# Optimization experiments

Measured on AMD Instinct MI355X. Metric: run time of the kernel, lower is better.

Reference implementation:

```python
import jax, jax.numpy as jnp
import numpy as np

N_NODES = 50000
N_EDGES = 800000
IN_FEATS = 128
HIDDEN = 256
N_CLASSES = 64


def setup_inputs() -> dict:
    key = jax.random.key(0)
    ks = jax.random.split(key, 16)
    def w(k, shape, fan_in):
        return jax.random.normal(k, shape, dtype=jnp.float32) * (1.0 / np.sqrt(fan_in))
    inp = {
        "x": jax.random.normal(ks[0], (N_NODES, IN_FEATS), dtype=jnp.float32),
        "edge_src": jax.random.randint(ks[1], (N_EDGES,), 0, N_NODES, dtype=jnp.int32),
        "edge_dst": jax.random.randint(ks[2], (N_EDGES,), 0, N_NODES, dtype=jnp.int32),
        # layer 0: in_feats -> hidden
        "W0s": w(ks[3], (IN_FEATS, HIDDEN), IN_FEATS),
        "W0n": w(ks[4], (IN_FEATS, HIDDEN), IN_FEATS),
        "b0": jnp.zeros((HIDDEN,), dtype=jnp.float32),
        # layer 1: hidden -> hidden
        "W1s": w(ks[5], (HIDDEN, HIDDEN), HIDDEN),
        "W1n": w(ks[6], (HIDDEN, HIDDEN), HIDDEN),
        "b1": jnp.zeros((HIDDEN,), dtype=jnp.float32),
        # layer 2: hidden -> hidden (last conv also outputs hidden per source code)
        "W2s": w(ks[7], (HIDDEN, HIDDEN), HIDDEN),
        "W2n": w(ks[8], (HIDDEN, HIDDEN), HIDDEN),
        "b2": jnp.zeros((HIDDEN,), dtype=jnp.float32),
        # fc1: hidden -> n_classes
        "Wfc": w(ks[9], (HIDDEN, N_CLASSES), HIDDEN),
        "bfc": jnp.zeros((N_CLASSES,), dtype=jnp.float32),
    }
    return inp


def _sage_layer(h, src, dst, Ws, Wn, b):
    # mean-neighbor aggregation: segment-sum messages, divide by in-degree
    msg = h[src]  # [E, D] irregular gather
    agg = jax.ops.segment_sum(msg, dst, num_segments=N_NODES)  # [N, D]
    deg = jax.ops.segment_sum(jnp.ones_like(dst, dtype=h.dtype), dst, num_segments=N_NODES)
    h_neigh = agg / jnp.maximum(deg, 1.0)[:, None]
    # DGL SAGEConv (mean): fc_self(h) + fc_neigh(h_neigh) + bias
    return h @ Ws + h_neigh @ Wn + b


def reference(x, edge_src, edge_dst, W0s, W0n, b0, W1s, W1n, b1, W2s, W2n, b2, Wfc, bfc):
    # forward applies dropout (identity at eval) and NO activation between layers,
    # matching the original module's forward().
    h = _sage_layer(x, edge_src, edge_dst, W0s, W0n, b0)
    h = _sage_layer(h, edge_src, edge_dst, W1s, W1n, b1)
    h = _sage_layer(h, edge_src, edge_dst, W2s, W2n, b2)
    return h @ Wfc + bfc  # [N, n_classes]
```

## Files before the change

kernel.cpp:

```cpp
#include <hip/hip_runtime.h>

#define NN 50000
#define NE 800000
#define F_IN 128
#define HID 256
#define N_CLS 64
#define SCAN_BLOCKS ((NN + 255) / 256)
#define CROWS 515

typedef _Float16 half8 __attribute__((ext_vector_type(8)));
typedef float f32x4 __attribute__((ext_vector_type(4)));

__global__ void hist_count(const int* __restrict__ dst, int* __restrict__ cnt,
                           unsigned short* __restrict__ rank, int E) {
    int i = blockIdx.x * blockDim.x + threadIdx.x;
    if (i < E) rank[i] = (unsigned short)atomicAdd(&cnt[dst[i]], 1);
}

__device__ __forceinline__ void scan_block_sums_dev(const int* __restrict__ cnt,
                                                    int* __restrict__ blockSums, int n) {
    __shared__ int s[256];
    int t = threadIdx.x;
    int i = blockIdx.x * 256 + t;
    s[t] = (i < n) ? cnt[i] : 0;
    __syncthreads();
    for (int off = 128; off > 0; off >>= 1) {
        if (t < off) s[t] += s[t + off];
        __syncthreads();
    }
    if (t == 0) blockSums[blockIdx.x] = s[0];
}

__device__ __forceinline__ void scan_top_dev(int* __restrict__ blockSums, int nb) {
    __shared__ int s[256];
    int t = threadIdx.x;
    s[t] = (t < nb) ? blockSums[t] : 0;
    __syncthreads();
    for (int off = 1; off < 256; off <<= 1) {
        int v = (t >= off) ? s[t - off] : 0;
        __syncthreads();
        s[t] += v;
        __syncthreads();
    }
    if (t < nb) blockSums[t] = (t > 0) ? s[t - 1] : 0;
}

__device__ __forceinline__ void scan_final_dev(const int* __restrict__ cnt,
                                               const int* __restrict__ blockBase,
                                               int* __restrict__ offs,
                                               float* __restrict__ dinv, int n) {
    __shared__ int s[256];
    int t = threadIdx.x;
    int i = blockIdx.x * 256 + t;
    int v = (i < n) ? cnt[i] : 0;
    s[t] = v;
    __syncthreads();
    for (int off = 1; off < 256; off <<= 1) {
        int u = (t >= off) ? s[t - off] : 0;
        __syncthreads();
        s[t] += u;
        __syncthreads();
    }
    if (i < n) {
        offs[i] = blockBase[blockIdx.x] + s[t] - v;
        dinv[i] = 1.0f / (float)max(v, 1);
    }
    if (i == n - 1) offs[n] = blockBase[blockIdx.x] + s[t];
}

__global__ void csr_place2(const int* __restrict__ src, const int* __restrict__ dst,
                           const unsigned short* __restrict__ rank, const int* __restrict__ offs,
                           unsigned short* __restrict__ csr, int E) {
    int e = blockIdx.x * blockDim.x + threadIdx.x;
    if (e < E) csr[offs[dst[e]] + rank[e]] = (unsigned short)src[e];
}

__device__ __forceinline__ const float* virtC1_row(int r, const float* W0s,
                                                   const float* W0n, const float* b0) {
    if (r < 0) return nullptr;
    if (r < 128) return W0s + (size_t)r * 256;
    if (r < 256) return W0n + (size_t)(r - 128) * 256;
    if (r == 512) return b0;
    return nullptr;
}

__device__ __forceinline__ int shift_src(int r) {
    if (r >= 128 && r < 512) return r - 128;
    if (r == 513) return 512;
    if (r == 514) return 513;
    return -1;
}


__device__ __forceinline__ void compose_first_dev(
    int bx, const float* __restrict__ W0s, const float* __restrict__ W0n,
    const float* __restrict__ b0,
    const float* __restrict__ B1, const float* __restrict__ B2,
    const float* __restrict__ brow, float* __restrict__ C)
{
    __shared__ float As[64][17];
    __shared__ float Bs[16][64];
    const int tid = threadIdx.x;
    const int tx = tid & 15, ty = tid >> 4;
    const int row0 = (bx % 9) * 64;
    const int col0 = (bx / 9) * 64;
    const int lr = tid >> 2, lc = tid & 3;
    const int br = tid >> 4, bc = tid & 15;

    float acc[4][4] = {};

    for (int pass = 0; pass < 2; ++pass) {
        const float* B = pass ? B2 : B1;
        int grow = row0 + lr;
        int srcr = pass ? shift_src(grow) : (grow < CROWS ? grow : -1);
        const float* ap = virtC1_row(srcr, W0s, W0n, b0);

        for (int k0 = 0; k0 < 256; k0 += 16) {
            float4 av = make_float4(0.f, 0.f, 0.f, 0.f);
            if (ap) av = *(const float4*)(ap + k0 + lc * 4);
            As[lr][lc * 4 + 0] = av.x;
            As[lr][lc * 4 + 1] = av.y;
            As[lr][lc * 4 + 2] = av.z;
            As[lr][lc * 4 + 3] = av.w;
            *(float4*)&Bs[br][bc * 4] = *(const float4*)(B + (size_t)(k0 + br) * 256 + col0 + bc * 4);
            __syncthreads();
            #pragma unroll
            for (int k = 0; k < 16; ++k) {
                float a[4];
                #pragma unroll
                for (int i = 0; i < 4; ++i) a[i] = As[ty * 4 + i][k];
                float4 bv = *(const float4*)&Bs[k][tx * 4];
                const float b[4] = {bv.x, bv.y, bv.z, bv.w};
                #pragma unroll
                for (int i = 0; i < 4; ++i)
                    #pragma unroll
                    for (int j = 0; j < 4; ++j)
                        acc[i][j] += a[i] * b[j];
            }
            __syncthreads();
        }
    }

    #pragma unroll
    for (int i = 0; i < 4; ++i) {
        int r = row0 + ty * 4 + i;
        if (r < CROWS) {
            #pragma unroll
            for (int j = 0; j < 4; ++j) {
                float v = acc[i][j];
                if (r == 512) v += brow[col0 + tx * 4 + j];
                C[(size_t)r * 256 + col0 + tx * 4 + j] = v;
            }
        }
    }
}

__device__ __forceinline__ void compose_mid_dev(
    int bx, const float* __restrict__ A,
    const float* __restrict__ B1, const float* __restrict__ B2,
    const float* __restrict__ brow, float* __restrict__ C)
{
    __shared__ float As[64][17];
    __shared__ float Bs[16][64];
    const int tid = threadIdx.x;
    const int tx = tid & 15, ty = tid >> 4;
    const int row0 = (bx % 9) * 64;
    const int col0 = (bx / 9) * 64;
    const int lr = tid >> 2, lc = tid & 3;
    const int br = tid >> 4, bc = tid & 15;

    float acc[4][4] = {};

    for (int pass = 0; pass < 2; ++pass) {
        const float* B = pass ? B2 : B1;
        int grow = row0 + lr;
        int p = pass ? shift_src(grow) : (grow < CROWS ? grow : -1);

        for (int k0 = 0; k0 < 256; k0 += 16) {
            float4 av = make_float4(0.f, 0.f, 0.f, 0.f);
            if (p >= 0) av = *(const float4*)(A + (size_t)p * 256 + k0 + lc * 4);
            As[lr][lc * 4 + 0] = av.x;
            As[lr][lc * 4 + 1] = av.y;
            As[lr][lc * 4 + 2] = av.z;
            As[lr][lc * 4 + 3] = av.w;
            *(float4*)&Bs[br][bc * 4] = *(const float4*)(B + (size_t)(k0 + br) * 256 + col0 + bc * 4);
            __syncthreads();
            #pragma unroll
            for (int k = 0; k < 16; ++k) {
                float a[4];
                #pragma unroll
                for (int i = 0; i < 4; ++i) a[i] = As[ty * 4 + i][k];
                float4 bv = *(const float4*)&Bs[k][tx * 4];
                const float b[4] = {bv.x, bv.y, bv.z, bv.w};
                #pragma unroll
                for (int i = 0; i < 4; ++i)
                    #pragma unroll
                    for (int j = 0; j < 4; ++j)
                        acc[i][j] += a[i] * b[j];
            }
            __syncthreads();
        }
    }

    #pragma unroll
    for (int i = 0; i < 4; ++i) {
        int r = row0 + ty * 4 + i;
        if (r < CROWS) {
            #pragma unroll
            for (int j = 0; j < 4; ++j) {
                float v = acc[i][j];
                if (r == 512) v += brow[col0 + tx * 4 + j];
                C[(size_t)r * 256 + col0 + tx * 4 + j] = v;
            }
        }
    }
}

__device__ __forceinline__ void compose_last_dev(
    int bx, const float* __restrict__ A, const float* __restrict__ B1,
    const float* __restrict__ brow, float* __restrict__ Vf, _Float16* __restrict__ BT)
{
    __shared__ float As[64][17];
    __shared__ float Bs[16][64];
    const int tid = threadIdx.x;
    const int tx = tid & 15, ty = tid >> 4;
    const int row0 = bx * 64;
    const int lr = tid >> 2, lc = tid & 3;
    const int br = tid >> 4, bc = tid & 15;

    float acc[4][4] = {};

    for (int k0 = 0; k0 < 256; k0 += 16) {
        float4 av = make_float4(0.f, 0.f, 0.f, 0.f);
        int grow = row0 + lr;
        if (grow < CROWS) av = *(const float4*)(A + (size_t)grow * 256 + k0 + lc * 4);
        As[lr][lc * 4 + 0] = av.x;
        As[lr][lc * 4 + 1] = av.y;
        As[lr][lc * 4 + 2] = av.z;
        As[lr][lc * 4 + 3] = av.w;
        *(float4*)&Bs[br][bc * 4] = *(const float4*)(B1 + (size_t)(k0 + br) * 64 + bc * 4);
        __syncthreads();
        #pragma unroll
        for (int k = 0; k < 16; ++k) {
            float a[4];
            #pragma unroll
            for (int i = 0; i < 4; ++i) a[i] = As[ty * 4 + i][k];
            float4 bv = *(const float4*)&Bs[k][tx * 4];
            const float b[4] = {bv.x, bv.y, bv.z, bv.w};
            #pragma unroll
            for (int i = 0; i < 4; ++i)
                #pragma unroll
                for (int j = 0; j < 4; ++j)
                    acc[i][j] += a[i] * b[j];
        }
        __syncthreads();
    }

    #pragma unroll
    for (int i = 0; i < 4; ++i) {
        int r = row0 + ty * 4 + i;
        if (r < CROWS) {
            #pragma unroll
            for (int j = 0; j < 4; ++j) {
                int c = tx * 4 + j;
                float v = acc[i][j];
                if (r == 512) v += brow[c];
                Vf[(size_t)r * 64 + c] = v;
                if (r < 512)
                    BT[(size_t)((r >> 7) * 64 + c) * 128 + (r & 127)] = (_Float16)v;
            }
        }
    }
}

__global__ __launch_bounds__(256) void k_scanA_composeF(
    const int* __restrict__ cnt, int* __restrict__ blockSums,
    const float* __restrict__ W0s, const float* __restrict__ W0n, const float* __restrict__ b0,
    const float* __restrict__ W1s, const float* __restrict__ W1n, const float* __restrict__ b1,
    float* __restrict__ C2)
{
    if (blockIdx.x < SCAN_BLOCKS) scan_block_sums_dev(cnt, blockSums, NN);
    else compose_first_dev(blockIdx.x - SCAN_BLOCKS, W0s, W0n, b0, W1s, W1n, b1, C2);
}

__global__ __launch_bounds__(256) void k_scanT_composeM(
    int* __restrict__ blockSums,
    const float* __restrict__ C2,
    const float* __restrict__ W2s, const float* __restrict__ W2n, const float* __restrict__ b2,
    float* __restrict__ C3)
{
    if (blockIdx.x == 0) scan_top_dev(blockSums, SCAN_BLOCKS);
    else compose_mid_dev(blockIdx.x - 1, C2, W2s, W2n, b2, C3);
}

__global__ __launch_bounds__(256) void k_scanF_composeL(
    const int* __restrict__ cnt, const int* __restrict__ blockBase,
    int* __restrict__ offs, float* __restrict__ dinv,
    const float* __restrict__ C3, const float* __restrict__ Wfc, const float* __restrict__ bfc,
    float* __restrict__ Vf, _Float16* __restrict__ BT)
{
    if (blockIdx.x < SCAN_BLOCKS) scan_final_dev(cnt, blockBase, offs, dinv, NN);
    else compose_last_dev(blockIdx.x - SCAN_BLOCKS, C3, Wfc, bfc, Vf, BT);
}

__global__ __launch_bounds__(256) void gemm_Y(
    const float* __restrict__ X, const _Float16* __restrict__ BT,
    _Float16* __restrict__ Y, _Float16* __restrict__ Tc, int N)
{
    constexpr int LP = 40;
    __shared__ _Float16 As[128 * LP];
    __shared__ _Float16 Bs[128 * LP];

    const int tid = threadIdx.x;
    const int wave = tid >> 6;
    const int lane = tid & 63;
    const int l15 = lane & 15;
    const int quad = lane >> 4;
    const int wrow = wave >> 1;
    const int wcol = wave & 1;
    const int m_base = wrow * 64;
    const int n_base = wcol * 64;

    const int row0 = blockIdx.x * 128;
    const int col0 = blockIdx.y * 128;

    f32x4 acc[4][4] = {};

    for (int k0 = 0; k0 < 128; k0 += 32) {
        #pragma unroll
        for (int r = 0; r < 2; ++r) {
            int idx = r * 256 + tid;
            int row = idx >> 2, ch = idx & 3;
            int gr = row0 + row; if (gr > N - 1) gr = N - 1;
            const float* ap = X + (size_t)gr * 128 + k0 + ch * 8;
            float4 f0 = *(const float4*)ap;
            float4 f1 = *(const float4*)(ap + 4);
            half8 v = { (_Float16)f0.x, (_Float16)f0.y, (_Float16)f0.z, (_Float16)f0.w,
                        (_Float16)f1.x, (_Float16)f1.y, (_Float16)f1.z, (_Float16)f1.w };
            *(half8*)&As[row * LP + ch * 8] = v;
        }
        #pragma unroll
        for (int r = 0; r < 2; ++r) {
            int idx = r * 256 + tid;
            int row = idx >> 2, ch = idx & 3;
            *(half8*)&Bs[row * LP + ch * 8] =
                *(const half8*)(BT + (size_t)(col0 + row) * 128 + k0 + ch * 8);
        }
        __syncthreads();
        half8 af[4], bf[4];
        #pragma unroll
        for (int i = 0; i < 4; ++i)
            af[i] = *(const half8*)&As[(m_base + i * 16 + l15) * LP + quad * 8];
        #pragma unroll
        for (int j = 0; j < 4; ++j)
            bf[j] = *(const half8*)&Bs[(n_base + j * 16 + l15) * LP + quad * 8];
        #pragma unroll
        for (int i = 0; i < 4; ++i)
            #pragma unroll
            for (int j = 0; j < 4; ++j)
                acc[i][j] = __builtin_amdgcn_mfma_f32_16x16x32_f16(af[i], bf[j], acc[i][j], 0, 0, 0);
        __syncthreads();
    }

    #pragma unroll
    for (int i = 0; i < 4; ++i) {
        #pragma unroll
        for (int j = 0; j < 4; ++j) {
            int col = col0 + n_base + j * 16 + l15;
            #pragma unroll
            for (int r = 0; r < 4; ++r) {
                int row = row0 + m_base + i * 16 + quad * 4 + r;
                if (row < N) {
                    _Float16 v = (_Float16)acc[i][j][r];
                    Y[(size_t)row * 256 + col] = v;
                    if (col >= 192) Tc[(size_t)row * 64 + (col - 192)] = v;
                }
            }
        }
    }
}

template <bool OUT_F32>
__global__ __launch_bounds__(256) void gather64(
    const _Float16* __restrict__ Tin,
    const unsigned short* __restrict__ csr, const int* __restrict__ offs,
    const float* __restrict__ dinv,
    const _Float16* __restrict__ Yadd,
    const float* __restrict__ cvec,
    void* __restrict__ Tout, int N)
{
    int node = blockIdx.x * 32 + (threadIdx.x >> 3);
    int lane = threadIdx.x & 7;
    if (node >= N) return;
    int beg = offs[node], end = offs[node + 1];
    float acc[8] = {};
    int e = beg;
    for (; e + 3 < end; e += 4) {
        int s0 = csr[e], s1 = csr[e + 1], s2 = csr[e + 2], s3 = csr[e + 3];
        half8 v0 = *(const half8*)(Tin + (size_t)s0 * 64 + lane * 8);
        half8 v1 = *(const half8*)(Tin + (size_t)s1 * 64 + lane * 8);
        half8 v2 = *(const half8*)(Tin + (size_t)s2 * 64 + lane * 8);
        half8 v3 = *(const half8*)(Tin + (size_t)s3 * 64 + lane * 8);
        #pragma unroll
        for (int j = 0; j < 8; ++j)
            acc[j] += ((float)v0[j] + (float)v1[j]) + ((float)v2[j] + (float)v3[j]);
    }
    for (; e < end; ++e) {
        half8 v = *(const half8*)(Tin + (size_t)csr[e] * 64 + lane * 8);
        #pragma unroll
        for (int j = 0; j < 8; ++j) acc[j] += (float)v[j];
    }
    float sc = dinv[node];
    half8 y = *(const half8*)(Yadd + (size_t)node * 256 + lane * 8);
    if (OUT_F32) {
        float* o = (float*)Tout + (size_t)node * 64 + lane * 8;
        float4 o0, o1;
        o0.x = acc[0] * sc + (float)y[0] + cvec[lane * 8 + 0];
        o0.y = acc[1] * sc + (float)y[1] + cvec[lane * 8 + 1];
        o0.z = acc[2] * sc + (float)y[2] + cvec[lane * 8 + 2];
        o0.w = acc[3] * sc + (float)y[3] + cvec[lane * 8 + 3];
        o1.x = acc[4] * sc + (float)y[4] + cvec[lane * 8 + 4];
        o1.y = acc[5] * sc + (float)y[5] + cvec[lane * 8 + 5];
        o1.z = acc[6] * sc + (float)y[6] + cvec[lane * 8 + 6];
        o1.w = acc[7] * sc + (float)y[7] + cvec[lane * 8 + 7];
        *(float4*)o = o0;
        *(float4*)(o + 4) = o1;
    } else {
        half8 o;
        #pragma unroll
        for (int j = 0; j < 8; ++j)
            o[j] = (_Float16)(acc[j] * sc + (float)y[j] + cvec[lane * 8 + j]);
        *(half8*)((_Float16*)Tout + (size_t)node * 64 + lane * 8) = o;
    }
}

extern "C" void kernel_launch(void* const* d_in, const int* in_sizes, int n_in,
                              void* d_out, int out_size, void* d_ws, size_t ws_size,
                              hipStream_t stream) {
    const float* x    = (const float*)d_in[0];
    const int*   esrc = (const int*)d_in[1];
    const int*   edst = (const int*)d_in[2];
    const float* W0s  = (const float*)d_in[3];
    const float* W0n  = (const float*)d_in[4];
    const float* b0   = (const float*)d_in[5];
    const float* W1s  = (const float*)d_in[6];
    const float* W1n  = (const float*)d_in[7];
    const float* b1   = (const float*)d_in[8];
    const float* W2s  = (const float*)d_in[9];
    const float* W2n  = (const float*)d_in[10];
    const float* b2   = (const float*)d_in[11];
    const float* Wfc  = (const float*)d_in[12];
    const float* bfc  = (const float*)d_in[13];
    float* out = (float*)d_out;

    _Float16* Y   = (_Float16*)d_ws;
    _Float16* Ta  = Y + (size_t)NN * 256;
    _Float16* Tb  = Ta + (size_t)NN * 64;
    _Float16* Tc  = Tb + (size_t)NN * 64;
    _Float16* BT  = Tc + (size_t)NN * 64;
    float* C2     = (float*)(BT + 256 * 128);
    float* C3     = C2 + CROWS * 256;
    float* Vf     = C3 + CROWS * 256;
    float* dinv   = Vf + CROWS * 64;
    int* cnt      = (int*)(dinv + NN);
    int* offs     = cnt + NN;
    int* blockSums = offs + NN + 1;
    unsigned short* rank = (unsigned short*)(blockSums + SCAN_BLOCKS);
    unsigned short* csr  = rank + NE;

    hipMemsetAsync(cnt, 0, (size_t)NN * sizeof(int), stream);
    hist_count<<<(NE + 255) / 256, 256, 0, stream>>>(edst, cnt, rank, NE);
    k_scanA_composeF<<<SCAN_BLOCKS + 36, 256, 0, stream>>>(
        cnt, blockSums, W0s, W0n, b0, W1s, W1n, b1, C2);
    k_scanT_composeM<<<1 + 36, 256, 0, stream>>>(blockSums, C2, W2s, W2n, b2, C3);
    k_scanF_composeL<<<SCAN_BLOCKS + 9, 256, 0, stream>>>(
        cnt, blockSums, offs, dinv, C3, Wfc, bfc, Vf, BT);
    csr_place2<<<(NE + 255) / 256, 256, 0, stream>>>(esrc, edst, rank, offs, csr, NE);

    gemm_Y<<<dim3((NN + 127) / 128, 2), 256, 0, stream>>>(x, BT, Y, Tc, NN);

    const int ggrid = (NN + 31) / 32;
    gather64<false><<<ggrid, 256, 0, stream>>>(
        Tc, csr, offs, dinv, Y + 128, Vf + (size_t)514 * 64, Ta, NN);
    gather64<false><<<ggrid, 256, 0, stream>>>(
        Ta, csr, offs, dinv, Y + 64, Vf + (size_t)513 * 64, Tb, NN);
    gather64<true><<<ggrid, 256, 0, stream>>>(
        Tb, csr, offs, dinv, Y, Vf + (size_t)512 * 64, out, NN);
}
```

Baseline: 291.9 us.

## Reschedule setup stages into fused launches and run gathers in one cooperative kernel

Reorders the preprocessing pipeline so the histogram overlaps the first weight composition, and the scan stages overlap the remaining compose and the split GEMM. The CSR placement is merged with the second GEMM half. The three gather layers are replaced by a single cooperative grid-stride kernel with grid-wide syncs, falling back to separate launches if the cooperative launch fails. This removes several kernel launches and their boundaries, but the grid syncs and the fixed grid size (256 CUs times occupancy) may cost load balance and occupancy.

```diff
diff --git a/kernel.cpp b/kernel.cpp
--- a/kernel.cpp
+++ b/kernel.cpp
@@ -1,4 +1,7 @@
 #include <hip/hip_runtime.h>
+#include <hip/hip_cooperative_groups.h>
+
+namespace cg = cooperative_groups;
 
 #define NN 50000
 #define NE 800000
@@ -6,74 +9,14 @@
 #define HID 256
 #define N_CLS 64
 #define SCAN_BLOCKS ((NN + 255) / 256)
+#define HB ((NE + 255) / 256)
+#define CF_BLOCKS 36
+#define CL_BLOCKS 9
+#define GA_BLOCKS ((NN + 127) / 128)
 #define CROWS 515
 
 typedef _Float16 half8 __attribute__((ext_vector_type(8)));
 typedef float f32x4 __attribute__((ext_vector_type(4)));
-
-__global__ void hist_count(const int* __restrict__ dst, int* __restrict__ cnt,
-                           unsigned short* __restrict__ rank, int E) {
-    int i = blockIdx.x * blockDim.x + threadIdx.x;
-    if (i < E) rank[i] = (unsigned short)atomicAdd(&cnt[dst[i]], 1);
-}
-
-__device__ __forceinline__ void scan_block_sums_dev(const int* __restrict__ cnt,
-                                                    int* __restrict__ blockSums, int n) {
-    __shared__ int s[256];
-    int t = threadIdx.x;
-    int i = blockIdx.x * 256 + t;
-    s[t] = (i < n) ? cnt[i] : 0;
-    __syncthreads();
-    for (int off = 128; off > 0; off >>= 1) {
-        if (t < off) s[t] += s[t + off];
-        __syncthreads();
-    }
-    if (t == 0) blockSums[blockIdx.x] = s[0];
-}
-
-__device__ __forceinline__ void scan_top_dev(int* __restrict__ blockSums, int nb) {
-    __shared__ int s[256];
-    int t = threadIdx.x;
-    s[t] = (t < nb) ? blockSums[t] : 0;
-    __syncthreads();
-    for (int off = 1; off < 256; off <<= 1) {
-        int v = (t >= off) ? s[t - off] : 0;
-        __syncthreads();
-        s[t] += v;
-        __syncthreads();
-    }
-    if (t < nb) blockSums[t] = (t > 0) ? s[t - 1] : 0;
-}
-
-__device__ __forceinline__ void scan_final_dev(const int* __restrict__ cnt,
-                                               const int* __restrict__ blockBase,
-                                               int* __restrict__ offs,
-                                               float* __restrict__ dinv, int n) {
-    __shared__ int s[256];
-    int t = threadIdx.x;
-    int i = blockIdx.x * 256 + t;
-    int v = (i < n) ? cnt[i] : 0;
-    s[t] = v;
-    __syncthreads();
-    for (int off = 1; off < 256; off <<= 1) {
-        int u = (t >= off) ? s[t - off] : 0;
-        __syncthreads();
-        s[t] += u;
-        __syncthreads();
-    }
-    if (i < n) {
-        offs[i] = blockBase[blockIdx.x] + s[t] - v;
-        dinv[i] = 1.0f / (float)max(v, 1);
-    }
-    if (i == n - 1) offs[n] = blockBase[blockIdx.x] + s[t];
-}
-
-__global__ void csr_place2(const int* __restrict__ src, const int* __restrict__ dst,
-                           const unsigned short* __restrict__ rank, const int* __restrict__ offs,
-                           unsigned short* __restrict__ csr, int E) {
-    int e = blockIdx.x * blockDim.x + threadIdx.x;
-    if (e < E) csr[offs[dst[e]] + rank[e]] = (unsigned short)src[e];
-}
 
 __device__ __forceinline__ const float* virtC1_row(int r, const float* W0s,
                                                    const float* W0n, const float* b0) {
@@ -90,7 +33,6 @@
     if (r == 514) return 513;
     return -1;
 }
-
 
 __device__ __forceinline__ void compose_first_dev(
     int bx, const float* __restrict__ W0s, const float* __restrict__ W0n,
@@ -273,37 +215,59 @@
     }
 }
 
-__global__ __launch_bounds__(256) void k_scanA_composeF(
-    const int* __restrict__ cnt, int* __restrict__ blockSums,
-    const float* __restrict__ W0s, const float* __restrict__ W0n, const float* __restrict__ b0,
-    const float* __restrict__ W1s, const float* __restrict__ W1n, const float* __restrict__ b1,
-    float* __restrict__ C2)
-{
-    if (blockIdx.x < SCAN_BLOCKS) scan_block_sums_dev(cnt, blockSums, NN);
-    else compose_first_dev(blockIdx.x - SCAN_BLOCKS, W0s, W0n, b0, W1s, W1n, b1, C2);
-}
-
-__global__ __launch_bounds__(256) void k_scanT_composeM(
-    int* __restrict__ blockSums,
-    const float* __restrict__ C2,
-    const float* __restrict__ W2s, const float* __restrict__ W2n, const float* __restrict__ b2,
-    float* __restrict__ C3)
-{
-    if (blockIdx.x == 0) scan_top_dev(blockSums, SCAN_BLOCKS);
-    else compose_mid_dev(blockIdx.x - 1, C2, W2s, W2n, b2, C3);
-}
-
-__global__ __launch_bounds__(256) void k_scanF_composeL(
-    const int* __restrict__ cnt, const int* __restrict__ blockBase,
-    int* __restrict__ offs, float* __restrict__ dinv,
-    const float* __restrict__ C3, const float* __restrict__ Wfc, const float* __restrict__ bfc,
-    float* __restrict__ Vf, _Float16* __restrict__ BT)
-{
-    if (blockIdx.x < SCAN_BLOCKS) scan_final_dev(cnt, blockBase, offs, dinv, NN);
-    else compose_last_dev(blockIdx.x - SCAN_BLOCKS, C3, Wfc, bfc, Vf, BT);
-}
-
-__global__ __launch_bounds__(256) void gemm_Y(
+__device__ __forceinline__ void scan_block_sums_dev(const int* __restrict__ cnt,
+                                                    int* __restrict__ blockSums, int n, int bx) {
+    __shared__ int s[256];
+    int t = threadIdx.x;
+    int i = bx * 256 + t;
+    s[t] = (i < n) ? cnt[i] : 0;
+    __syncthreads();
+    for (int off = 128; off > 0; off >>= 1) {
+        if (t < off) s[t] += s[t + off];
+        __syncthreads();
+    }
+    if (t == 0) blockSums[bx] = s[0];
+}
+
+__device__ __forceinline__ void scan_top_dev(int* __restrict__ blockSums, int nb) {
+    __shared__ int s[256];
+    int t = threadIdx.x;
+    s[t] = (t < nb) ? blockSums[t] : 0;
+    __syncthreads();
+    for (int off = 1; off < 256; off <<= 1) {
+        int v = (t >= off) ? s[t - off] : 0;
+        __syncthreads();
+        s[t] += v;
+        __syncthreads();
+    }
+    if (t < nb) blockSums[t] = (t > 0) ? s[t - 1] : 0;
+}
+
+__device__ __forceinline__ void scan_final_dev(const int* __restrict__ cnt,
+                                               const int* __restrict__ blockBase,
+                                               int* __restrict__ offs,
+                                               float* __restrict__ dinv, int n, int bx) {
+    __shared__ int s[256];
+    int t = threadIdx.x;
+    int i = bx * 256 + t;
+    int v = (i < n) ? cnt[i] : 0;
+    s[t] = v;
+    __syncthreads();
+    for (int off = 1; off < 256; off <<= 1) {
+        int u = (t >= off) ? s[t - off] : 0;
+        __syncthreads();
+        s[t] += u;
+        __syncthreads();
+    }
+    if (i < n) {
+        offs[i] = blockBase[bx] + s[t] - v;
+        dinv[i] = 1.0f / (float)max(v, 1);
+    }
+    if (i == n - 1) offs[n] = blockBase[bx] + s[t];
+}
+
+__device__ __forceinline__ void gemm_y_dev(
+    int bx, int by,
     const float* __restrict__ X, const _Float16* __restrict__ BT,
     _Float16* __restrict__ Y, _Float16* __restrict__ Tc, int N)
 {
@@ -321,8 +285,8 @@
     const int m_base = wrow * 64;
     const int n_base = wcol * 64;
 
-    const int row0 = blockIdx.x * 128;
-    const int col0 = blockIdx.y * 128;
+    const int row0 = bx * 128;
+    const int col0 = by * 128;
 
     f32x4 acc[4][4] = {};
 
@@ -380,18 +344,74 @@
     }
 }
 
+__global__ __launch_bounds__(256) void k_composeF_hist(
+    const int* __restrict__ edst, int* __restrict__ cnt, unsigned short* __restrict__ rank,
+    const float* __restrict__ W0s, const float* __restrict__ W0n, const float* __restrict__ b0,
+    const float* __restrict__ W1s, const float* __restrict__ W1n, const float* __restrict__ b1,
+    float* __restrict__ C2)
+{
+    if (blockIdx.x < CF_BLOCKS) {
+        compose_first_dev(blockIdx.x, W0s, W0n, b0, W1s, W1n, b1, C2);
+    } else {
+        int e = (blockIdx.x - CF_BLOCKS) * 256 + threadIdx.x;
+        if (e < NE) rank[e] = (unsigned short)atomicAdd(&cnt[edst[e]], 1);
+    }
+}
+
+__global__ __launch_bounds__(256) void k_composeM_scanA(
+    const int* __restrict__ cnt, int* __restrict__ blockSums,
+    const float* __restrict__ C2,
+    const float* __restrict__ W2s, const float* __restrict__ W2n, const float* __restrict__ b2,
+    float* __restrict__ C3)
+{
+    if (blockIdx.x < CF_BLOCKS) compose_mid_dev(blockIdx.x, C2, W2s, W2n, b2, C3);
+    else scan_block_sums_dev(cnt, blockSums, NN, blockIdx.x - CF_BLOCKS);
+}
+
+__global__ __launch_bounds__(256) void k_scanT_composeL(
+    int* __restrict__ blockSums,
+    const float* __restrict__ C3, const float* __restrict__ Wfc, const float* __restrict__ bfc,
+    float* __restrict__ Vf, _Float16* __restrict__ BT)
+{
+    if (blockIdx.x == 0) scan_top_dev(blockSums, SCAN_BLOCKS);
+    else compose_last_dev(blockIdx.x - 1, C3, Wfc, bfc, Vf, BT);
+}
+
+__global__ __launch_bounds__(256) void k_gemmA_scanF(
+    const int* __restrict__ cnt, const int* __restrict__ blockBase,
+    int* __restrict__ offs, float* __restrict__ dinv,
+    const float* __restrict__ X, const _Float16* __restrict__ BT,
+    _Float16* __restrict__ Y, _Float16* __restrict__ Tc)
+{
+    if (blockIdx.x < GA_BLOCKS) gemm_y_dev(blockIdx.x, 0, X, BT, Y, Tc, NN);
+    else scan_final_dev(cnt, blockBase, offs, dinv, NN, blockIdx.x - GA_BLOCKS);
+}
+
+__global__ __launch_bounds__(256) void k_gemmB_place(
+    const int* __restrict__ esrc, const int* __restrict__ edst,
+    const unsigned short* __restrict__ rank, const int* __restrict__ offs,
+    unsigned short* __restrict__ csr,
+    const float* __restrict__ X, const _Float16* __restrict__ BT,
+    _Float16* __restrict__ Y, _Float16* __restrict__ Tc)
+{
+    if (blockIdx.x < GA_BLOCKS) {
+        gemm_y_dev(blockIdx.x, 1, X, BT, Y, Tc, NN);
+    } else {
+        int e = (blockIdx.x - GA_BLOCKS) * 256 + threadIdx.x;
+        if (e < NE) csr[offs[edst[e]] + rank[e]] = (unsigned short)esrc[e];
+    }
+}
+
 template <bool OUT_F32>
-__global__ __launch_bounds__(256) void gather64(
+__device__ __forceinline__ void gather_node_dev(
+    int node, int lane,
     const _Float16* __restrict__ Tin,
     const unsigned short* __restrict__ csr, const int* __restrict__ offs,
     const float* __restrict__ dinv,
     const _Float16* __restrict__ Yadd,
     const float* __restrict__ cvec,
-    void* __restrict__ Tout, int N)
-{
-    int node = blockIdx.x * 32 + (threadIdx.x >> 3);
-    int lane = threadIdx.x & 7;
-    if (node >= N) return;
+    void* __restrict__ Tout)
+{
     int beg = offs[node], end = offs[node + 1];
     float acc[8] = {};
     int e = beg;
@@ -432,6 +452,55 @@
             o[j] = (_Float16)(acc[j] * sc + (float)y[j] + cvec[lane * 8 + j]);
         *(half8*)((_Float16*)Tout + (size_t)node * 64 + lane * 8) = o;
     }
+}
+
+__global__ __launch_bounds__(256, 6) void coop_gather(
+    const _Float16* __restrict__ Tc, _Float16* __restrict__ Ta, _Float16* __restrict__ Tb,
+    const unsigned short* __restrict__ csr, const int* __restrict__ offs,
+    const float* __restrict__ dinv, const _Float16* __restrict__ Y,
+    const float* __restrict__ Vf, float* __restrict__ out)
+{
+    cg::grid_group grid = cg::this_grid();
+    const int g = threadIdx.x >> 3;
+    const int lane = threadIdx.x & 7;
+
+    for (int base = blockIdx.x * 32; base < NN; base += gridDim.x * 32) {
+        int node = base + g;
+        if (node < NN)
+            gather_node_dev<false>(node, lane, Tc, csr, offs, dinv,
+                                   Y + 128, Vf + (size_t)514 * 64, (void*)Ta);
+    }
+    __threadfence();
+    grid.sync();
+    for (int base = blockIdx.x * 32; base < NN; base += gridDim.x * 32) {
+        int node = base + g;
+        if (node < NN)
+            gather_node_dev<false>(node, lane, Ta, csr, offs, dinv,
+                                   Y + 64, Vf + (size_t)513 * 64, (void*)Tb);
+    }
+    __threadfence();
+    grid.sync();
+    for (int base = blockIdx.x * 32; base < NN; base += gridDim.x * 32) {
+        int node = base + g;
+        if (node < NN)
+            gather_node_dev<true>(node, lane, Tb, csr, offs, dinv,
+                                  Y, Vf + (size_t)512 * 64, (void*)out);
+    }
+}
+
+template <bool OUT_F32>
+__global__ __launch_bounds__(256) void gather64(
+    const _Float16* __restrict__ Tin,
+    const unsigned short* __restrict__ csr, const int* __restrict__ offs,
+    const float* __restrict__ dinv,
+    const _Float16* __restrict__ Yadd,
+    const float* __restrict__ cvec,
+    void* __restrict__ Tout, int N)
+{
+    int node = blockIdx.x * 32 + (threadIdx.x >> 3);
+    int lane = threadIdx.x & 7;
+    if (node >= N) return;
+    gather_node_dev<OUT_F32>(node, lane, Tin, csr, offs, dinv, Yadd, cvec, Tout);
 }
 
 extern "C" void kernel_launch(void* const* d_in, const int* in_sizes, int n_in,
@@ -469,21 +538,45 @@
     unsigned short* csr  = rank + NE;
 
     hipMemsetAsync(cnt, 0, (size_t)NN * sizeof(int), stream);
-    hist_count<<<(NE + 255) / 256, 256, 0, stream>>>(edst, cnt, rank, NE);
-    k_scanA_composeF<<<SCAN_BLOCKS + 36, 256, 0, stream>>>(
-        cnt, blockSums, W0s, W0n, b0, W1s, W1n, b1, C2);
-    k_scanT_composeM<<<1 + 36, 256, 0, stream>>>(blockSums, C2, W2s, W2n, b2, C3);
-    k_scanF_composeL<<<SCAN_BLOCKS + 9, 256, 0, stream>>>(
-        cnt, blockSums, offs, dinv, C3, Wfc, bfc, Vf, BT);
-    csr_place2<<<(NE + 255) / 256, 256, 0, stream>>>(esrc, edst, rank, offs, csr, NE);
-
-    gemm_Y<<<dim3((NN + 127) / 128, 2), 256, 0, stream>>>(x, BT, Y, Tc, NN);
-
-    const int ggrid = (NN + 31) / 32;
-    gather64<false><<<ggrid, 256, 0, stream>>>(
-        Tc, csr, offs, dinv, Y + 128, Vf + (size_t)514 * 64, Ta, NN);
-    gather64<false><<<ggrid, 256, 0, stream>>>(
-        Ta, csr, offs, dinv, Y + 64, Vf + (size_t)513 * 64, Tb, NN);
-    gather64<true><<<ggrid, 256, 0, stream>>>(
-        Tb, csr, offs, dinv, Y, Vf + (size_t)512 * 64, out, NN);
-}
+
+    k_composeF_hist<<<CF_BLOCKS + HB, 256, 0, stream>>>(
+        edst, cnt, rank, W0s, W0n, b0, W1s, W1n, b1, C2);
+
+    k_composeM_scanA<<<CF_BLOCKS + SCAN_BLOCKS, 256, 0, stream>>>(
+        cnt, blockSums, C2, W2s, W2n, b2, C3);
+
+    k_scanT_composeL<<<1 + CL_BLOCKS, 256, 0, stream>>>(
+        blockSums, C3, Wfc, bfc, Vf, BT);
+
+    k_gemmA_scanF<<<GA_BLOCKS + SCAN_BLOCKS, 256, 0, stream>>>(
+        cnt, blockSums, offs, dinv, x, BT, Y, Tc);
+
+    k_gemmB_place<<<GA_BLOCKS + HB, 256, 0, stream>>>(
+        esrc, edst, rank, offs, csr, x, BT, Y, Tc);
+
+    static int coopb = 0;
+    if (coopb == 0) {
+        int maxb = 0;
+        if (hipOccupancyMaxActiveBlocksPerMultiprocessor(&maxb, coop_gather, 256, 0) != hipSuccess
+            || maxb < 1) maxb = 1;
+        if (maxb > 8) maxb = 8;
+        coopb = 256 * maxb;
+    }
+    {
+        const _Float16* a0 = Tc; _Float16* a1 = Ta; _Float16* a2 = Tb;
+        const unsigned short* a3 = csr; const int* a4 = offs; const float* a5 = dinv;
+        const _Float16* a6 = Y; const float* a7 = Vf; float* a8 = out;
+        void* kargs[] = {&a0, &a1, &a2, &a3, &a4, &a5, &a6, &a7, &a8};
+        hipError_t ce = hipLaunchCooperativeKernel(
+            coop_gather, dim3(coopb), dim3(256), kargs, 0, stream);
+        if (ce != hipSuccess) {
+            const int ggrid = (NN + 31) / 32;
+            gather64<false><<<ggrid, 256, 0, stream>>>(
+                Tc, csr, offs, dinv, Y + 128, Vf + (size_t)514 * 64, (void*)Ta, NN);
+            gather64<false><<<ggrid, 256, 0, stream>>>(
+                Ta, csr, offs, dinv, Y + 64, Vf + (size_t)513 * 64, (void*)Tb, NN);
+            gather64<true><<<ggrid, 256, 0, stream>>>(
+                Tb, csr, offs, dinv, Y, Vf + (size_t)512 * 64, (void*)out, NN);
+        }
+    }
+}
```

Measured after the change: 763.9 us. 162% more time.
